# Kernel optimization log

Measured on AMD Instinct MI355X. Metric: run time of the kernel, lower is better.

Reference implementation:

```python
import jax, jax.numpy as jnp
import numpy as np

SEQ_LEN = 2048
NUM_GLOBAL = 32
NEG_INF = float('-inf')


def _build_mask(seq_len=SEQ_LEN, num_global=NUM_GLOBAL):
    # Causal mask: triu(ones).T == lower-triangular ones; zeros -> -inf, ones -> 0.
    m = np.where(np.tril(np.ones((seq_len, seq_len), dtype=np.float32)) == 1.0, 0.0, NEG_INF)
    # Deterministic 'random.sample' of global tokens (fixed for reproducibility).
    rng = np.random.default_rng(0)
    gtok = rng.choice(seq_len, size=num_global, replace=False)
    m[:, gtok] = 0.0
    m[gtok, :] = 0.0
    return jnp.asarray(m)


def setup_inputs() -> dict:
    key = jax.random.key(0)
    ks = jax.random.split(key, 9)
    B, S, D_IN, D_QK = 8, SEQ_LEN, 1024, 128
    return {
        'q': jax.random.normal(ks[0], (B, S, D_IN), dtype=jnp.float32),
        'k': jax.random.normal(ks[1], (B, S, D_IN), dtype=jnp.float32),
        'v': jax.random.normal(ks[2], (B, S, D_IN), dtype=jnp.float32),
        'Wq': jax.random.normal(ks[3], (D_QK, D_IN), dtype=jnp.float32) * 0.02,
        'bq': jax.random.normal(ks[4], (D_QK,), dtype=jnp.float32) * 0.02,
        'Wk': jax.random.normal(ks[5], (D_QK, D_IN), dtype=jnp.float32) * 0.02,
        'bk': jax.random.normal(ks[6], (D_QK,), dtype=jnp.float32) * 0.02,
        'Wv': jax.random.normal(ks[7], (D_QK, D_IN), dtype=jnp.float32) * 0.02,
        'bv': jax.random.normal(ks[8], (D_QK,), dtype=jnp.float32) * 0.02,
    }


def reference(q, k, v, Wq, bq, Wk, bk, Wv, bv):
    # Linear projections (torch nn.Linear: x @ W.T + b)
    Q = jnp.einsum('bsd,qd->bsq', q, Wq) + bq   # [B,S,dq]
    K = jnp.einsum('bsd,qd->bsq', k, Wk) + bk   # [B,S,dk]
    V = jnp.einsum('bsd,qd->bsq', v, Wv) + bv   # [B,S,dk]
    mask = _build_mask()                        # [S,S] static causal+global
    scale = K.shape[-1] ** 0.5
    scores = jnp.einsum('bqd,bkd->bqk', Q, K)   # dense QK^T [B,S,S]
    scores = (scores + mask) / scale            # (-inf stays -inf)
    attn = jax.nn.softmax(scores, axis=-1)
    return jnp.einsum('bqk,bkd->bqd', attn, V)
```

## Files before the change

kernel.cpp:

```cpp
#include <hip/hip_runtime.h>
#include <cstdint>

constexpr int SEQ  = 2048;
constexpr int DIN  = 1024;
constexpr int DQK  = 128;
constexpr int NB   = 8;
constexpr int MTOT = NB * SEQ;
constexpr float INV_SCALE = 0.08838834764831845f;

typedef __attribute__((ext_vector_type(8))) short  short8;
typedef __attribute__((ext_vector_type(4))) float  floatx4;
typedef __attribute__((ext_vector_type(4))) int    intx4;

struct GM { unsigned long long w[32]; };

static void compute_gtok(unsigned long long bits[32]) {
  typedef unsigned __int128 u128;
  uint32_t pool[4];
  uint32_t hc = 0x43b0d7e5u;
  auto hashmix = [&hc](uint32_t v) -> uint32_t {
    v ^= hc; hc *= 0x931e8875u; v *= hc; v ^= v >> 16; return v;
  };
  auto mixf = [](uint32_t x, uint32_t y) -> uint32_t {
    uint32_t r = x * 0xca01f9ddu - y * 0x4973f715u;
    r ^= r >> 16; return r;
  };
  pool[0] = hashmix(0u);
  for (int i = 1; i < 4; ++i) pool[i] = hashmix(0u);
  for (int s = 0; s < 4; ++s)
    for (int d = 0; d < 4; ++d)
      if (s != d) pool[d] = mixf(pool[d], hashmix(pool[s]));
  uint32_t hb = 0x8b51f9ddu;
  uint32_t st[8];
  for (int i = 0; i < 8; ++i) {
    uint32_t dv = pool[i & 3];
    dv ^= hb; hb *= 0x58f38dedu; dv *= hb; dv ^= dv >> 16;
    st[i] = dv;
  }
  uint64_t sv[4];
  for (int i = 0; i < 4; ++i)
    sv[i] = (uint64_t)st[2 * i] | ((uint64_t)st[2 * i + 1] << 32);
  const u128 MUL = ((u128)2549297995355413924ULL << 64) | (u128)4865540595714422341ULL;
  u128 initstate = ((u128)sv[0] << 64) | sv[1];
  u128 initseq   = ((u128)sv[2] << 64) | sv[3];
  u128 state = 0;
  u128 inc = (initseq << 1) | 1;
  state = state * MUL + inc;
  state += initstate;
  state = state * MUL + inc;
  bool has32 = false; uint32_t cache32 = 0;
  auto next64 = [&]() -> uint64_t {
    state = state * MUL + inc;
    uint64_t hi = (uint64_t)(state >> 64);
    uint64_t lo = (uint64_t)state;
    unsigned rot = (unsigned)(state >> 122);
    uint64_t x = hi ^ lo;
    return (x >> rot) | (x << ((64u - rot) & 63u));
  };
  auto next32 = [&]() -> uint32_t {
    if (has32) { has32 = false; return cache32; }
    uint64_t n = next64();
    has32 = true; cache32 = (uint32_t)(n >> 32);
    return (uint32_t)n;
  };
  bool in_set[SEQ];
  for (int i = 0; i < SEQ; ++i) in_set[i] = false;
  for (uint32_t j = 2016; j < 2048; ++j) {
    uint32_t rng_excl = j + 1;
    uint64_t m = (uint64_t)next32() * rng_excl;
    uint32_t leftover = (uint32_t)m;
    if (leftover < rng_excl) {
      uint32_t threshold = (0xFFFFFFFFu - j) % rng_excl;
      while (leftover < threshold) {
        m = (uint64_t)next32() * rng_excl;
        leftover = (uint32_t)m;
      }
    }
    uint32_t val = (uint32_t)(m >> 32);
    if (in_set[val]) in_set[j] = true;
    else in_set[val] = true;
  }
  for (int i = 0; i < 32; ++i) bits[i] = 0ULL;
  for (int t = 0; t < SEQ; ++t)
    if (in_set[t]) bits[t >> 6] |= (1ULL << (t & 63));
}

__device__ __forceinline__ void ldsld16(const void* g, void* l) {
  __builtin_amdgcn_global_load_lds(
      (const __attribute__((address_space(1))) unsigned int*)g,
      (__attribute__((address_space(3))) unsigned int*)l, 16, 0, 0);
}
__device__ __forceinline__ bool gbit(const GM& g, int j) {
  return (g.w[j >> 6] >> (j & 63)) & 1ULL;
}
__device__ __forceinline__ void split4(float4 x, unsigned hw[2], unsigned lw[2]) {
  unsigned u0 = __float_as_uint(x.x), u1 = __float_as_uint(x.y);
  unsigned u2 = __float_as_uint(x.z), u3 = __float_as_uint(x.w);
  hw[0] = __builtin_amdgcn_perm(u1, u0, 0x07060302u);
  hw[1] = __builtin_amdgcn_perm(u3, u2, 0x07060302u);
  unsigned r0 = __float_as_uint(x.x - __uint_as_float(u0 & 0xFFFF0000u));
  unsigned r1 = __float_as_uint(x.y - __uint_as_float(u1 & 0xFFFF0000u));
  unsigned r2 = __float_as_uint(x.z - __uint_as_float(u2 & 0xFFFF0000u));
  unsigned r3 = __float_as_uint(x.w - __uint_as_float(u3 & 0xFFFF0000u));
  lw[0] = __builtin_amdgcn_perm(r1, r0, 0x07060302u);
  lw[1] = __builtin_amdgcn_perm(r3, r2, 0x07060302u);
}
__device__ __forceinline__ void split1(float v, unsigned short& h, unsigned short& l) {
  unsigned u = __float_as_uint(v);
  h = (unsigned short)(u >> 16);
  float rr = v - __uint_as_float(u & 0xFFFF0000u);
  l = (unsigned short)(__float_as_uint(rr) >> 16);
}
__device__ __forceinline__ unsigned short bfr_rne(float v) {
  unsigned u = __float_as_uint(v);
  return (unsigned short)((u + 0x7FFFu + ((u >> 16) & 1u)) >> 16);
}

__global__ __launch_bounds__(256) void wconv_kernel(
    const float* __restrict__ Wq, const float* __restrict__ Wk, const float* __restrict__ Wv,
    unsigned short* __restrict__ Whi, unsigned short* __restrict__ Wlo) {
  const float* W = blockIdx.y == 0 ? Wq : blockIdx.y == 1 ? Wk : Wv;
  size_t base = (size_t)blockIdx.y * DQK * DIN;
  int e = (blockIdx.x * 256 + threadIdx.x) * 4;
  float4 x = *(const float4*)&W[e];
  unsigned hw[2], lw[2];
  split4(x, hw, lw);
  *(uint2*)&Whi[base + e] = make_uint2(hw[0], hw[1]);
  *(uint2*)&Wlo[base + e] = make_uint2(lw[0], lw[1]);
}

__global__ __launch_bounds__(256, 3) void proj_kernel(
    const float* __restrict__ xq, const float* __restrict__ xk, const float* __restrict__ xv,
    const unsigned short* __restrict__ Whi, const unsigned short* __restrict__ Wlo,
    const float* __restrict__ bq, const float* __restrict__ bk, const float* __restrict__ bv,
    unsigned short* __restrict__ Qb, unsigned short* __restrict__ Kb,
    unsigned short* __restrict__ Vth) {
  const int which = blockIdx.y;
  const float* X    = which == 0 ? xq : which == 1 ? xk : xv;
  const float* bias = which == 0 ? bq : which == 1 ? bk : bv;
  const int m0 = blockIdx.x * 64;

  __shared__ __align__(16) unsigned char LDSb[49152];

  const int tid = threadIdx.x;
  const int w = tid >> 6, lane = tid & 63, l15 = lane & 15, quad = lane >> 4;
  const int mh = (w >> 1) * 32, nh = (w & 1) * 64;

  floatx4 acc[2][4] = {};
  float biasv[4];
#pragma unroll
  for (int j = 0; j < 4; ++j) biasv[j] = bias[nh + j * 16 + l15];

  const unsigned short* WhiP = Whi + (size_t)which * DQK * DIN;
  const unsigned short* WloP = Wlo + (size_t)which * DQK * DIN;

  const char* gp[6];
  unsigned    ldsoff[6];
#pragma unroll
  for (int i = 0; i < 6; ++i) {
    if (i < 2) {
      int cx = w + 4 * i;
      int R  = cx * 8 + (lane >> 3);
      int sg = (lane & 7) ^ (R & 7);
      gp[i] = (const char*)(X + (size_t)(m0 + R) * DIN + sg * 4);
      ldsoff[i] = cx * 1024;
    } else {
      int ii = (i < 4) ? i - 2 : i - 4;
      int cw = w + 4 * ii;
      int n  = cw * 16 + (lane >> 2);
      int sg = (lane & 3) ^ (n & 3);
      const unsigned short* Wp = (i < 4) ? WhiP : WloP;
      gp[i] = (const char*)(Wp + (size_t)n * DIN + sg * 8);
      ldsoff[i] = ((i < 4) ? 16384u : 32768u) + cw * 1024;
    }
  }

  auto stage = [&](int nb) {
#pragma unroll
    for (int i = 0; i < 6; ++i) {
      ldsld16(gp[i], LDSb + ldsoff[i] + nb * 8192);
      gp[i] += (i < 2) ? 128 : 64;
    }
  };

  int buf = 0;
  stage(0);
  __syncthreads();

  for (int it = 0; it < 32; ++it) {
    if (it + 1 < 32) stage(buf ^ 1);

    const float*          Xs  = (const float*)(LDSb + buf * 8192);
    const unsigned short* WhS = (const unsigned short*)(LDSb + 16384 + buf * 8192);
    const unsigned short* WlS = (const unsigned short*)(LDSb + 32768 + buf * 8192);

    short8 Ah[2], Al[2];
#pragma unroll
    for (int ms = 0; ms < 2; ++ms) {
      int R = mh + ms * 16 + l15;
      const float* row = Xs + R * 32;
      float4 xa = *(const float4*)&row[((2 * quad) ^ (R & 7)) * 4];
      float4 xb = *(const float4*)&row[((2 * quad + 1) ^ (R & 7)) * 4];
      unsigned ha[2], la[2], hb2[2], lb2[2];
      split4(xa, ha, la);
      split4(xb, hb2, lb2);
      union { short8 v; unsigned u[4]; } H, L;
      H.u[0] = ha[0]; H.u[1] = ha[1]; H.u[2] = hb2[0]; H.u[3] = hb2[1];
      L.u[0] = la[0]; L.u[1] = la[1]; L.u[2] = lb2[0]; L.u[3] = lb2[1];
      Ah[ms] = H.v; Al[ms] = L.v;
    }
    short8 Bh[4], Bl[4];
#pragma unroll
    for (int ns = 0; ns < 4; ++ns) {
      int n = nh + ns * 16 + l15;
      int off = n * 32 + ((quad ^ (n & 3)) * 8);
      Bh[ns] = *(const short8*)&WhS[off];
      Bl[ns] = *(const short8*)&WlS[off];
    }
#pragma unroll
    for (int i = 0; i < 2; ++i)
#pragma unroll
      for (int j = 0; j < 4; ++j) {
        floatx4 c = acc[i][j];
        c = __builtin_amdgcn_mfma_f32_16x16x32_bf16(Ah[i], Bh[j], c, 0, 0, 0);
        c = __builtin_amdgcn_mfma_f32_16x16x32_bf16(Ah[i], Bl[j], c, 0, 0, 0);
        c = __builtin_amdgcn_mfma_f32_16x16x32_bf16(Al[i], Bh[j], c, 0, 0, 0);
        acc[i][j] = c;
      }

    __syncthreads();
    buf ^= 1;
  }

  if (which < 2) {
    unsigned short* O = which == 0 ? Qb : Kb;
#pragma unroll
    for (int i = 0; i < 2; ++i)
#pragma unroll
      for (int j = 0; j < 4; ++j)
#pragma unroll
        for (int r = 0; r < 4; ++r) {
          int m = mh + i * 16 + quad * 4 + r;
          int n = nh + j * 16 + l15;
          O[(size_t)(m0 + m) * DQK + n] = bfr_rne(acc[i][j][r] + biasv[j]);
        }
  } else {
    __syncthreads();
    unsigned short* VH = (unsigned short*)LDSb;
#pragma unroll
    for (int i = 0; i < 2; ++i)
#pragma unroll
      for (int j = 0; j < 4; ++j)
#pragma unroll
        for (int r = 0; r < 4; ++r) {
          int s = mh + i * 16 + quad * 4 + r;
          int d = nh + j * 16 + l15;
          VH[d * 64 + (((s >> 3) ^ (d & 7)) * 8) + (s & 7)] =
              bfr_rne(acc[i][j][r] + biasv[j]);
        }
    __syncthreads();
    int b = m0 >> 11, s0 = m0 & 2047;
#pragma unroll
    for (int i = 0; i < 4; ++i) {
      int cch = i * 256 + tid;
      int d = cch >> 3, gI = cch & 7;
      int loff = d * 64 + ((gI ^ (d & 7)) * 8);
      intx4 vh = *(const intx4*)&VH[loff];
      *(intx4*)&Vth[((size_t)b * DQK + d) * SEQ + s0 + gI * 8] = vh;
    }
  }
}

__global__ __launch_bounds__(256, 3) void attn_kernel(
    const unsigned short* __restrict__ Qb, const unsigned short* __restrict__ Kb,
    const unsigned short* __restrict__ Vth,
    float* __restrict__ Opart, float2* __restrict__ ML, GM g, unsigned int t64) {
  __shared__ unsigned short Ks[64 * 128];
  __shared__ unsigned short Vh[128 * 64];
  __shared__ unsigned short Ph[4][16 * 72];
  __shared__ unsigned short Pl[4][16 * 72];

  const int tid = threadIdx.x;
  const int w = tid >> 6, lane = tid & 63, l15 = lane & 15, quad = lane >> 4;
  const int b = blockIdx.y;
  const int qt = blockIdx.x / 3, s3 = blockIdx.x - qt * 3;
  const int qs = qt * 64;

  short8 qf[4];
  const unsigned short* Qrow = Qb + ((size_t)(b * SEQ + qs + w * 16 + l15)) * DQK;
#pragma unroll
  for (int j = 0; j < 4; ++j) qf[j] = *(const short8*)&Qrow[j * 32 + quad * 8];

  int rowi[4]; bool growb[4];
#pragma unroll
  for (int r = 0; r < 4; ++r) {
    rowi[r] = qs + w * 16 + quad * 4 + r;
    growb[r] = gbit(g, rowi[r]);
  }

  floatx4 o[8] = {};
  float m_r[4] = {-1e30f, -1e30f, -1e30f, -1e30f};
  float l_r[4] = {0.f, 0.f, 0.f, 0.f};

  const bool qhasg = (t64 >> qt) & 1;
  const unsigned short* KbB = Kb  + (size_t)b * SEQ * DQK;
  const unsigned short* VhB = Vth + (size_t)b * DQK * SEQ;

  for (int kt = s3; kt < 32; kt += 3) {
    const int ks0 = kt * 64;
    if (!((ks0 <= qs + 63) || ((t64 >> kt) & 1) || qhasg)) continue;

    __syncthreads();
#pragma unroll
    for (int i = 0; i < 8; ++i) {
      int c = w * 8 + i;
      if (c < 16) {
        int F = c * 1024 + lane * 16;
        int r = F >> 8, gs = (F >> 4) & 15, gl = gs ^ (r & 15);
        ldsld16(KbB + (size_t)(ks0 + r) * DQK + gl * 8, (char*)Ks + c * 1024);
      } else {
        int cc = c - 16;
        int F = cc * 1024 + lane * 16;
        int d = F >> 7, gs = (F >> 4) & 7, gl = gs ^ (d & 7);
        ldsld16(VhB + (size_t)d * SEQ + ks0 + gl * 8, (char*)Vh + cc * 1024);
      }
    }
    __syncthreads();

    floatx4 S[4];
#pragma unroll
    for (int c4 = 0; c4 < 4; ++c4) {
      floatx4 s = {0.f, 0.f, 0.f, 0.f};
#pragma unroll
      for (int j = 0; j < 4; ++j) {
        short8 kf = *(const short8*)&Ks[(c4 * 16 + l15) * 128 + (((j * 4 + quad) ^ l15) * 8)];
        s = __builtin_amdgcn_mfma_f32_16x16x32_bf16(qf[j], kf, s, 0, 0, 0);
      }
      S[c4] = s;
    }

    float z[4][4];
    float mx[4] = {-1e30f, -1e30f, -1e30f, -1e30f};
#pragma unroll
    for (int c4 = 0; c4 < 4; ++c4) {
      int col = ks0 + c4 * 16 + l15;
      bool cg = gbit(g, col);
#pragma unroll
      for (int r = 0; r < 4; ++r) {
        bool ok = (col <= rowi[r]) || cg || growb[r];
        float zz = ok ? S[c4][r] * INV_SCALE : -1e30f;
        z[c4][r] = zz;
        mx[r] = fmaxf(mx[r], zz);
      }
    }
#pragma unroll
    for (int d = 1; d < 16; d <<= 1)
#pragma unroll
      for (int r = 0; r < 4; ++r) mx[r] = fmaxf(mx[r], __shfl_xor(mx[r], d));
    float alpha[4], rs[4] = {0.f, 0.f, 0.f, 0.f};
#pragma unroll
    for (int r = 0; r < 4; ++r) {
      float mn = fmaxf(m_r[r], mx[r]);
      alpha[r] = __expf(m_r[r] - mn);
      m_r[r] = mn;
    }
    float p[4][4];
#pragma unroll
    for (int c4 = 0; c4 < 4; ++c4)
#pragma unroll
      for (int r = 0; r < 4; ++r) {
        float pp = __expf(z[c4][r] - m_r[r]);
        p[c4][r] = pp;
        rs[r] += pp;
      }
#pragma unroll
    for (int d = 1; d < 16; d <<= 1)
#pragma unroll
      for (int r = 0; r < 4; ++r) rs[r] += __shfl_xor(rs[r], d);
#pragma unroll
    for (int r = 0; r < 4; ++r) l_r[r] = l_r[r] * alpha[r] + rs[r];
#pragma unroll
    for (int n = 0; n < 8; ++n)
#pragma unroll
      for (int r = 0; r < 4; ++r) o[n][r] *= alpha[r];

#pragma unroll
    for (int c4 = 0; c4 < 4; ++c4)
#pragma unroll
      for (int r = 0; r < 4; ++r) {
        unsigned short h, lo;
        split1(p[c4][r], h, lo);
        int off = (quad * 4 + r) * 72 + c4 * 16 + l15;
        Ph[w][off] = h; Pl[w][off] = lo;
      }
    short8 pf[2], pg[2];
#pragma unroll
    for (int kq = 0; kq < 2; ++kq) {
      int off = l15 * 72 + kq * 32 + quad * 8;
      pf[kq] = *(const short8*)&Ph[w][off];
      pg[kq] = *(const short8*)&Pl[w][off];
    }

#pragma unroll
    for (int n = 0; n < 8; ++n) {
      int drow = n * 16 + l15;
#pragma unroll
      for (int kq = 0; kq < 2; ++kq) {
        int off = drow * 64 + (((kq * 4 + quad) ^ (drow & 7)) * 8);
        short8 vhf = *(const short8*)&Vh[off];
        floatx4 c = o[n];
        c = __builtin_amdgcn_mfma_f32_16x16x32_bf16(pf[kq], vhf, c, 0, 0, 0);
        c = __builtin_amdgcn_mfma_f32_16x16x32_bf16(pg[kq], vhf, c, 0, 0, 0);
        o[n] = c;
      }
    }
  }

  const size_t grp = (size_t)(b * 32 + qt) * 3 + s3;
  float* Op = Opart + grp * 64 * 128;
#pragma unroll
  for (int n = 0; n < 8; ++n)
#pragma unroll
    for (int r = 0; r < 4; ++r)
      Op[(w * 16 + quad * 4 + r) * 128 + n * 16 + l15] = o[n][r];
  if (l15 == 0) {
#pragma unroll
    for (int r = 0; r < 4; ++r)
      ML[grp * 64 + w * 16 + quad * 4 + r] = make_float2(m_r[r], l_r[r]);
  }
}

__global__ __launch_bounds__(256) void merge_kernel(
    const float* __restrict__ Opart, const float2* __restrict__ ML,
    float* __restrict__ Out) {
  const int t = threadIdx.x;
  const int row = blockIdx.x * 2 + (t >> 7);
  const int col = t & 127;
  const int grp = row >> 6;
  const int rin = row & 63;
  const size_t base = (size_t)grp * 3;
  float2 ml0 = ML[(base + 0) * 64 + rin];
  float2 ml1 = ML[(base + 1) * 64 + rin];
  float2 ml2 = ML[(base + 2) * 64 + rin];
  const float m = fmaxf(fmaxf(ml0.x, ml1.x), ml2.x);
  const float w0 = __expf(ml0.x - m), w1 = __expf(ml1.x - m), w2 = __expf(ml2.x - m);
  const float denom = w0 * ml0.y + w1 * ml1.y + w2 * ml2.y;
  const float o0 = Opart[((base + 0) * 64 + rin) * 128 + col];
  const float o1 = Opart[((base + 1) * 64 + rin) * 128 + col];
  const float o2 = Opart[((base + 2) * 64 + rin) * 128 + col];
  Out[(size_t)row * 128 + col] = (w0 * o0 + w1 * o1 + w2 * o2) / denom;
}

extern "C" void kernel_launch(void* const* d_in, const int* in_sizes, int n_in,
                              void* d_out, int out_size, void* d_ws, size_t ws_size,
                              hipStream_t stream) {
  const float* q  = (const float*)d_in[0];
  const float* k  = (const float*)d_in[1];
  const float* v  = (const float*)d_in[2];
  const float* Wq = (const float*)d_in[3];
  const float* bq = (const float*)d_in[4];
  const float* Wk = (const float*)d_in[5];
  const float* bk = (const float*)d_in[6];
  const float* Wv = (const float*)d_in[7];
  const float* bv = (const float*)d_in[8];
  float* out = (float*)d_out;

  unsigned short* Qb  = (unsigned short*)d_ws;
  unsigned short* Kb2 = Qb  + (size_t)MTOT * DQK;
  unsigned short* Vth = Kb2 + (size_t)MTOT * DQK;
  unsigned short* Whi = Vth + (size_t)MTOT * DQK;
  unsigned short* Wlo = Whi + (size_t)3 * DQK * DIN;
  float*  Opart = (float*)(Wlo + (size_t)3 * DQK * DIN);
  float2* ML    = (float2*)(Opart + (size_t)3 * MTOT * DQK);

  GM g;
  compute_gtok(g.w);
  unsigned int t64 = 0;
  for (int t = 0; t < 32; ++t) if (g.w[t] != 0ULL) t64 |= (1u << t);

  hipLaunchKernelGGL(wconv_kernel, dim3(128, 3), dim3(256), 0, stream,
                     Wq, Wk, Wv, Whi, Wlo);
  hipLaunchKernelGGL(proj_kernel, dim3(256, 3), dim3(256), 0, stream,
                     q, k, v, Whi, Wlo, bq, bk, bv, Qb, Kb2, Vth);
  hipLaunchKernelGGL(attn_kernel, dim3(96, 8), dim3(256), 0, stream,
                     Qb, Kb2, Vth, Opart, ML, g, t64);
  hipLaunchKernelGGL(merge_kernel, dim3(MTOT / 2), dim3(256), 0, stream,
                     Opart, ML, out);
}
```

Measured before the change: 290.0 us.

## Replace double-buffered projection K-loop with single-buffer 64-wide K tiles

The projection kernel's K loop drops its double-buffered 32-wide staging and loads 64-wide K tiles into a single LDS buffer, with a barrier before and after each load. This halves the number of loop iterations and barriers and gives each tile twice the MFMA work, with swizzles widened to match the new row width. In exchange, global-to-LDS loads no longer overlap with compute, which may expose memory latency unless the three resident blocks per CU hide it.

```diff
diff --git a/kernel.cpp b/kernel.cpp
--- a/kernel.cpp
+++ b/kernel.cpp
@@ -141,6 +141,9 @@
   const int m0 = blockIdx.x * 64;
 
   __shared__ __align__(16) unsigned char LDSb[49152];
+  float*          Xs  = (float*)LDSb;
+  unsigned short* WhS = (unsigned short*)(LDSb + 16384);
+  unsigned short* WlS = (unsigned short*)(LDSb + 32768);
 
   const int tid = threadIdx.x;
   const int w = tid >> 6, lane = tid & 63, l15 = lane & 15, quad = lane >> 4;
@@ -154,82 +157,72 @@
   const unsigned short* WhiP = Whi + (size_t)which * DQK * DIN;
   const unsigned short* WloP = Wlo + (size_t)which * DQK * DIN;
 
-  const char* gp[6];
-  unsigned    ldsoff[6];
-#pragma unroll
-  for (int i = 0; i < 6; ++i) {
-    if (i < 2) {
-      int cx = w + 4 * i;
-      int R  = cx * 8 + (lane >> 3);
-      int sg = (lane & 7) ^ (R & 7);
+  const char* gp[12];
+  unsigned    ldsoff[12];
+#pragma unroll
+  for (int i = 0; i < 12; ++i) {
+    if (i < 4) {
+      int cx = w * 4 + i;
+      int R  = cx * 4 + (lane >> 4);
+      int sg = (lane & 15) ^ (R & 7);
       gp[i] = (const char*)(X + (size_t)(m0 + R) * DIN + sg * 4);
       ldsoff[i] = cx * 1024;
     } else {
-      int ii = (i < 4) ? i - 2 : i - 4;
-      int cw = w + 4 * ii;
-      int n  = cw * 16 + (lane >> 2);
-      int sg = (lane & 3) ^ (n & 3);
-      const unsigned short* Wp = (i < 4) ? WhiP : WloP;
+      int j  = (i < 8) ? i - 4 : i - 8;
+      int cw = w * 4 + j;
+      int n  = cw * 8 + (lane >> 3);
+      int sg = (lane & 7) ^ (n & 7);
+      const unsigned short* Wp = (i < 8) ? WhiP : WloP;
       gp[i] = (const char*)(Wp + (size_t)n * DIN + sg * 8);
-      ldsoff[i] = ((i < 4) ? 16384u : 32768u) + cw * 1024;
-    }
-  }
-
-  auto stage = [&](int nb) {
-#pragma unroll
-    for (int i = 0; i < 6; ++i) {
-      ldsld16(gp[i], LDSb + ldsoff[i] + nb * 8192);
-      gp[i] += (i < 2) ? 128 : 64;
-    }
-  };
-
-  int buf = 0;
-  stage(0);
-  __syncthreads();
-
-  for (int it = 0; it < 32; ++it) {
-    if (it + 1 < 32) stage(buf ^ 1);
-
-    const float*          Xs  = (const float*)(LDSb + buf * 8192);
-    const unsigned short* WhS = (const unsigned short*)(LDSb + 16384 + buf * 8192);
-    const unsigned short* WlS = (const unsigned short*)(LDSb + 32768 + buf * 8192);
-
-    short8 Ah[2], Al[2];
-#pragma unroll
-    for (int ms = 0; ms < 2; ++ms) {
-      int R = mh + ms * 16 + l15;
-      const float* row = Xs + R * 32;
-      float4 xa = *(const float4*)&row[((2 * quad) ^ (R & 7)) * 4];
-      float4 xb = *(const float4*)&row[((2 * quad + 1) ^ (R & 7)) * 4];
-      unsigned ha[2], la[2], hb2[2], lb2[2];
-      split4(xa, ha, la);
-      split4(xb, hb2, lb2);
-      union { short8 v; unsigned u[4]; } H, L;
-      H.u[0] = ha[0]; H.u[1] = ha[1]; H.u[2] = hb2[0]; H.u[3] = hb2[1];
-      L.u[0] = la[0]; L.u[1] = la[1]; L.u[2] = lb2[0]; L.u[3] = lb2[1];
-      Ah[ms] = H.v; Al[ms] = L.v;
-    }
-    short8 Bh[4], Bl[4];
-#pragma unroll
-    for (int ns = 0; ns < 4; ++ns) {
-      int n = nh + ns * 16 + l15;
-      int off = n * 32 + ((quad ^ (n & 3)) * 8);
-      Bh[ns] = *(const short8*)&WhS[off];
-      Bl[ns] = *(const short8*)&WlS[off];
-    }
-#pragma unroll
-    for (int i = 0; i < 2; ++i)
-#pragma unroll
-      for (int j = 0; j < 4; ++j) {
-        floatx4 c = acc[i][j];
-        c = __builtin_amdgcn_mfma_f32_16x16x32_bf16(Ah[i], Bh[j], c, 0, 0, 0);
-        c = __builtin_amdgcn_mfma_f32_16x16x32_bf16(Ah[i], Bl[j], c, 0, 0, 0);
-        c = __builtin_amdgcn_mfma_f32_16x16x32_bf16(Al[i], Bh[j], c, 0, 0, 0);
-        acc[i][j] = c;
-      }
-
-    __syncthreads();
-    buf ^= 1;
+      ldsoff[i] = ((i < 8) ? 16384u : 32768u) + cw * 1024;
+    }
+  }
+
+  for (int kb = 0; kb < DIN; kb += 64) {
+    __syncthreads();
+#pragma unroll
+    for (int i = 0; i < 12; ++i) {
+      ldsld16(gp[i], LDSb + ldsoff[i]);
+      gp[i] += (i < 4) ? 256 : 128;
+    }
+    __syncthreads();
+
+#pragma unroll
+    for (int ks = 0; ks < 2; ++ks) {
+      short8 Ah[2], Al[2], Bh[4], Bl[4];
+#pragma unroll
+      for (int ms = 0; ms < 2; ++ms) {
+        int R = mh + ms * 16 + l15;
+        const float* row = Xs + R * 64;
+        int g0 = ks * 8 + quad * 2;
+        float4 xa = *(const float4*)&row[(g0 ^ (R & 7)) * 4];
+        float4 xb = *(const float4*)&row[((g0 + 1) ^ (R & 7)) * 4];
+        unsigned ha[2], la[2], hb[2], lb[2];
+        split4(xa, ha, la);
+        split4(xb, hb, lb);
+        union { short8 v; unsigned u[4]; } H, L;
+        H.u[0] = ha[0]; H.u[1] = ha[1]; H.u[2] = hb[0]; H.u[3] = hb[1];
+        L.u[0] = la[0]; L.u[1] = la[1]; L.u[2] = lb[0]; L.u[3] = lb[1];
+        Ah[ms] = H.v; Al[ms] = L.v;
+      }
+#pragma unroll
+      for (int ns = 0; ns < 4; ++ns) {
+        int n = nh + ns * 16 + l15;
+        int off = n * 64 + (((ks * 4 + quad) ^ (n & 7)) * 8);
+        Bh[ns] = *(const short8*)&WhS[off];
+        Bl[ns] = *(const short8*)&WlS[off];
+      }
+#pragma unroll
+      for (int i = 0; i < 2; ++i)
+#pragma unroll
+        for (int j = 0; j < 4; ++j) {
+          floatx4 c = acc[i][j];
+          c = __builtin_amdgcn_mfma_f32_16x16x32_bf16(Ah[i], Bh[j], c, 0, 0, 0);
+          c = __builtin_amdgcn_mfma_f32_16x16x32_bf16(Ah[i], Bl[j], c, 0, 0, 0);
+          c = __builtin_amdgcn_mfma_f32_16x16x32_bf16(Al[i], Bh[j], c, 0, 0, 0);
+          acc[i][j] = c;
+        }
+    }
   }
 
   if (which < 2) {
```

Result: faster. 282.7 us (-2.5%).
